# Kernel optimization log

Measured on AMD Instinct MI355X. Metric: run time of the kernel, lower is better.

The kernel has to match this reference:

```python
import jax, jax.numpy as jnp
import numpy as np

NB_VARS = 2_000_000
N0 = 2 + 2 * NB_VARS      # input vector length: [zero, one, pos0, neg0, pos1, neg1, ...]
M0 = 4_000_000            # prod layer 0 outputs (binary fan-in)
M1 = 1_000_000            # sum  layer 1 outputs (irregular fan-in)
M2 = 500_000              # prod layer 2 outputs (binary fan-in)
M3 = 125_000              # sum  layer 3 outputs (irregular fan-in)


def setup_inputs() -> dict:
    key = jax.random.key(0)
    ks = jax.random.split(key, 7)
    x_pos = jax.random.uniform(ks[0], (NB_VARS,), dtype=jnp.float32)
    ix_in0 = jax.random.randint(ks[1], (2 * M0,), 0, N0)            # edges of prod layer 0
    ix_in1 = jax.random.randint(ks[2], (8_000_000,), 0, M0)         # edges of sum layer 1
    ix_out1 = jnp.sort(jax.random.randint(ks[3], (8_000_000,), 0, M1))
    ix_in2 = jax.random.randint(ks[4], (2 * M2,), 0, M1)            # edges of prod layer 2
    ix_in3 = jax.random.randint(ks[5], (1_000_000,), 0, M2)         # edges of sum layer 3
    ix_out3 = jnp.sort(jax.random.randint(ks[6], (1_000_000,), 0, M3))
    return {"x_pos": x_pos, "ix_in0": ix_in0, "ix_in1": ix_in1, "ix_out1": ix_out1,
            "ix_in2": ix_in2, "ix_in3": ix_in3, "ix_out3": ix_out3}


def reference(x_pos, ix_in0, ix_in1, ix_out1, ix_in2, ix_in3, ix_out3):
    # encode_input (real semiring): neg = negate(pos) = 1 - pos; interleave; prepend [zero=0, one=1]
    neg = 1.0 - x_pos
    units = jnp.array([0.0, 1.0], dtype=x_pos.dtype)
    x = jnp.concatenate([units, jnp.stack([x_pos, neg], axis=1).reshape(-1)])  # [N0]

    # layer 0: product layer, binary fan-in -> gather + pairwise multiply
    e0 = x[ix_in0].reshape(M0, 2)
    x = e0[:, 0] * e0[:, 1]                                                    # [M0]

    # layer 1: sum layer, irregular fan-in -> gather + segment-sum
    x = jax.ops.segment_sum(x[ix_in1], ix_out1, num_segments=M1)               # [M1]

    # layer 2: product layer, binary fan-in
    e2 = x[ix_in2].reshape(M2, 2)
    x = e2[:, 0] * e2[:, 1]                                                    # [M2]

    # layer 3: sum layer, irregular fan-in
    x = jax.ops.segment_sum(x[ix_in3], ix_out3, num_segments=M3)               # [M3]
    return x
```

## Files before the change

### kernel.cpp

```cpp
#include <hip/hip_runtime.h>
#include <hip/hip_fp16.h>


#define PERS_BLOCKS 2048
#define PERS_THREADS 256
#define WBITS_H 20

typedef __attribute__((ext_vector_type(4))) int   iv4;
typedef __attribute__((ext_vector_type(4))) float fv4;
typedef __attribute__((ext_vector_type(4))) unsigned int uv4;

__device__ __forceinline__ iv4 nt_load4(const int* p) {
    return __builtin_nontemporal_load((const iv4*)p);
}

__global__ void init_kernel(const float* __restrict__ in, unsigned int* __restrict__ x16,
                            float* __restrict__ y1, float* __restrict__ out,
                            int n4, int nz1, int nzo) {
    int t = blockIdx.x * blockDim.x + threadIdx.x;
    if (t < n4) {
        fv4 f = __builtin_nontemporal_load((const fv4*)(in + 4 * (size_t)t));
        __half2 lo = __floats2half2_rn(f.x, f.y);
        __half2 hi = __floats2half2_rn(f.z, f.w);
        unsigned int rlo = *(const unsigned int*)&lo;
        unsigned int rhi = *(const unsigned int*)&hi;
        x16[2 * t]     = rlo;
        x16[2 * t + 1] = rhi;
    }
    if (t < nz1) {
        fv4 z = {0.f, 0.f, 0.f, 0.f};
        __builtin_nontemporal_store(z, (fv4*)(y1 + 4 * (size_t)t));
    }
    if (t < nzo) {
        fv4 z = {0.f, 0.f, 0.f, 0.f};
        __builtin_nontemporal_store(z, (fv4*)(out + 4 * (size_t)t));
    }
}

__device__ __forceinline__ float decode16(const __half* __restrict__ xp, int idx) {
    int k = (idx - 2) >> 1;
    k = k < 0 ? 0 : k;
    float v = __half2float(xp[k]);
    v = (idx & 1) ? 1.0f - v : v;
    if (idx < 2) v = (float)idx;
    return v;
}

__global__ void layer0_prod8_kernel(const __half* __restrict__ x16,
                                    const int* __restrict__ ix,
                                    unsigned int* __restrict__ out16, int nT) {
    int t = blockIdx.x * blockDim.x + threadIdx.x;
    if (t >= nT) return;
    iv4 p0 = nt_load4(ix + 16 * (size_t)t);
    iv4 p1 = nt_load4(ix + 16 * (size_t)t + 4);
    iv4 p2 = nt_load4(ix + 16 * (size_t)t + 8);
    iv4 p3 = nt_load4(ix + 16 * (size_t)t + 12);
    float a0 = decode16(x16, p0.x), b0 = decode16(x16, p0.y);
    float a1 = decode16(x16, p0.z), b1 = decode16(x16, p0.w);
    float a2 = decode16(x16, p1.x), b2 = decode16(x16, p1.y);
    float a3 = decode16(x16, p1.z), b3 = decode16(x16, p1.w);
    float a4 = decode16(x16, p2.x), b4 = decode16(x16, p2.y);
    float a5 = decode16(x16, p2.z), b5 = decode16(x16, p2.w);
    float a6 = decode16(x16, p3.x), b6 = decode16(x16, p3.y);
    float a7 = decode16(x16, p3.z), b7 = decode16(x16, p3.w);
    __half2 h0 = __floats2half2_rn(a0 * b0, a1 * b1);
    __half2 h1 = __floats2half2_rn(a2 * b2, a3 * b3);
    __half2 h2 = __floats2half2_rn(a4 * b4, a5 * b5);
    __half2 h3 = __floats2half2_rn(a6 * b6, a7 * b7);
    uv4 r;
    r.x = *(const unsigned int*)&h0;
    r.y = *(const unsigned int*)&h1;
    r.z = *(const unsigned int*)&h2;
    r.w = *(const unsigned int*)&h3;
    __builtin_nontemporal_store(r, (uv4*)(out16 + 4 * (size_t)t));
}

template<int NS, int NWIN>
__global__ __launch_bounds__(PERS_THREADS)
void sum_win_h_kernel(const __half* __restrict__ vin,
                      const int* __restrict__ ix_in,
                      const int* __restrict__ ix_out,
                      float* __restrict__ out, int nT4) {
    const int nTh  = gridDim.x * blockDim.x;
    const int gtid = blockIdx.x * blockDim.x + threadIdx.x;
    const int lane = threadIdx.x & 63;

    iv4    a[NS];
    iv4    sg[NS];
    float4 v[NS];
    bool   act[NS];
    #pragma unroll
    for (int s = 0; s < NS; ++s) {
        int t = s * nTh + gtid;
        act[s] = (t < nT4);
        if (act[s]) {
            a[s]  = nt_load4(ix_in  + 4 * (size_t)t);
            sg[s] = nt_load4(ix_out + 4 * (size_t)t);
        } else {
            a[s]  = (iv4){-1, -1, -1, -1};
            sg[s] = (iv4){-1, -1, -1, -1};
        }
        v[s] = make_float4(0.f, 0.f, 0.f, 0.f);
    }

    #pragma unroll
    for (int w = 0; w < NWIN; ++w) {
        #pragma unroll
        for (int s = 0; s < NS; ++s) {
            if ((a[s].x >> WBITS_H) == w) v[s].x = __half2float(vin[a[s].x]);
            if ((a[s].y >> WBITS_H) == w) v[s].y = __half2float(vin[a[s].y]);
            if ((a[s].z >> WBITS_H) == w) v[s].z = __half2float(vin[a[s].z]);
            if ((a[s].w >> WBITS_H) == w) v[s].w = __half2float(vin[a[s].w]);
        }
    }

    #pragma unroll
    for (int s = 0; s < NS; ++s) {
        int seg = -1; float val = 0.f;
        if (act[s]) {
            int cur = sg[s].x; float acc = v[s].x;
            if (sg[s].y == cur) acc += v[s].y; else { atomicAdd(&out[cur], acc); cur = sg[s].y; acc = v[s].y; }
            if (sg[s].z == cur) acc += v[s].z; else { atomicAdd(&out[cur], acc); cur = sg[s].z; acc = v[s].z; }
            if (sg[s].w == cur) acc += v[s].w; else { atomicAdd(&out[cur], acc); cur = sg[s].w; acc = v[s].w; }
            seg = cur; val = acc;
        }
        #pragma unroll
        for (int off = 1; off < 64; off <<= 1) {
            float vv = __shfl_up(val, off, 64);
            int   ss = __shfl_up(seg, off, 64);
            if (lane >= off && ss == seg) val += vv;
        }
        int seg_next = __shfl_down(seg, 1, 64);
        bool is_last = (lane == 63) || (seg_next != seg);
        if (act[s] && is_last) atomicAdd(&out[seg], val);
    }
}

__global__ void sum4_f32_kernel(const float* __restrict__ vin,
                                const int* __restrict__ ix_in,
                                const int* __restrict__ ix_out,
                                float* __restrict__ out, int nT4) {
    int t = blockIdx.x * blockDim.x + threadIdx.x;
    int lane = threadIdx.x & 63;
    int seg = -1; float val = 0.f;
    if (t < nT4) {
        iv4 a  = nt_load4(ix_in  + 4 * (size_t)t);
        iv4 sg = nt_load4(ix_out + 4 * (size_t)t);
        float v0 = vin[a.x], v1 = vin[a.y], v2 = vin[a.z], v3 = vin[a.w];
        int cur = sg.x; float acc = v0;
        if (sg.y == cur) acc += v1; else { atomicAdd(&out[cur], acc); cur = sg.y; acc = v1; }
        if (sg.z == cur) acc += v2; else { atomicAdd(&out[cur], acc); cur = sg.z; acc = v2; }
        if (sg.w == cur) acc += v3; else { atomicAdd(&out[cur], acc); cur = sg.w; acc = v3; }
        seg = cur; val = acc;
    }
    #pragma unroll
    for (int off = 1; off < 64; off <<= 1) {
        float vv = __shfl_up(val, off, 64);
        int   ss = __shfl_up(seg, off, 64);
        if (lane >= off && ss == seg) val += vv;
    }
    int seg_next = __shfl_down(seg, 1, 64);
    bool is_last = (lane == 63) || (seg_next != seg);
    if (t < nT4 && is_last) atomicAdd(&out[seg], val);
}

__global__ void prod2_kernel(const float* __restrict__ vin,
                             const int* __restrict__ ix,
                             float2* __restrict__ out, int nT) {
    int t = blockIdx.x * blockDim.x + threadIdx.x;
    if (t >= nT) return;
    iv4 p = nt_load4(ix + 4 * (size_t)t);
    float a0 = vin[p.x], b0 = vin[p.y];
    float a1 = vin[p.z], b1 = vin[p.w];
    float2 r; r.x = a0 * b0; r.y = a1 * b1;
    out[t] = r;
}

extern "C" void kernel_launch(void* const* d_in, const int* in_sizes, int n_in,
                              void* d_out, int out_size, void* d_ws, size_t ws_size,
                              hipStream_t stream) {
    const float* x_pos  = (const float*)d_in[0];
    const int*   ix_in0 = (const int*)d_in[1];
    const int*   ix_in1 = (const int*)d_in[2];
    const int*   ix_out1= (const int*)d_in[3];
    const int*   ix_in2 = (const int*)d_in[4];
    const int*   ix_in3 = (const int*)d_in[5];
    const int*   ix_out3= (const int*)d_in[6];
    float* out = (float*)d_out;

    const int NV = in_sizes[0];
    const int M0 = in_sizes[1] / 2;
    const int E1 = in_sizes[2];
    const int M1 = 1000000;
    const int M2 = in_sizes[4] / 2;
    const int E3 = in_sizes[5];
    const int M3 = out_size;

    char* ws = (char*)d_ws;
    __half* y0  = (__half*)(ws);
    float*  y1  = (float*)(ws + (size_t)8  * 1024 * 1024);
    float*  y2  = (float*)(ws + (size_t)12 * 1024 * 1024);
    __half* x16 = (__half*)(ws + (size_t)14 * 1024 * 1024);

    const int B = 256;

    int n4  = NV / 4;
    int nz1 = M1 / 4;
    int nzo = M3 / 4;
    init_kernel<<<(n4 + B - 1) / B, B, 0, stream>>>(
        x_pos, (unsigned int*)x16, y1, out, n4, nz1, nzo);

    int t0 = M0 / 8;
    layer0_prod8_kernel<<<(t0 + B - 1) / B, B, 0, stream>>>(
        x16, ix_in0, (unsigned int*)y0, t0);

    int t1 = E1 / 4;
    sum_win_h_kernel<4, 4><<<PERS_BLOCKS, PERS_THREADS, 0, stream>>>(
        y0, ix_in1, ix_out1, y1, t1);

    int t2 = M2 / 2;
    prod2_kernel<<<(t2 + B - 1) / B, B, 0, stream>>>(
        y1, ix_in2, (float2*)y2, t2);

    int t3 = E3 / 4;
    sum4_f32_kernel<<<(t3 + B - 1) / B, B, 0, stream>>>(
        y2, ix_in3, ix_out3, out, t3);
}
```

Before: 252.6 us.

## Fuse all layers into one cooperative persistent kernel with grid syncs

Replaces the five separate kernel launches with a single cooperative mega-kernel that runs each layer as a grid-stride phase separated by grid.sync(). The aim is to remove per-launch overhead and the tail idle time between kernels. The original multi-launch path stays as a fallback if the cooperative launch fails. In exchange it adds grid-wide barrier costs, an occupancy query on every call, and fixed grid sizing for every phase, which may lower per-phase parallelism compared with the tuned launches.

Result: slower. 759.7 us (+200.7%).

```diff
diff --git a/kernel.cpp b/kernel.cpp
--- a/kernel.cpp
+++ b/kernel.cpp
@@ -1,9 +1,11 @@
 #include <hip/hip_runtime.h>
 #include <hip/hip_fp16.h>
-
-
-#define PERS_BLOCKS 2048
-#define PERS_THREADS 256
+#include <hip/hip_cooperative_groups.h>
+
+namespace cg = cooperative_groups;
+
+
+#define NTHR 256
 #define WBITS_H 20
 
 typedef __attribute__((ext_vector_type(4))) int   iv4;
@@ -12,6 +14,183 @@
 
 __device__ __forceinline__ iv4 nt_load4(const int* p) {
     return __builtin_nontemporal_load((const iv4*)p);
+}
+
+__device__ __forceinline__ float decode16(const __half* __restrict__ xp, int idx) {
+    int k = (idx - 2) >> 1;
+    k = k < 0 ? 0 : k;
+    float v = __half2float(xp[k]);
+    v = (idx & 1) ? 1.0f - v : v;
+    if (idx < 2) v = (float)idx;
+    return v;
+}
+
+__global__ __launch_bounds__(NTHR, 8)
+void mega_kernel(const float* __restrict__ x_pos,
+                 const int* __restrict__ ix_in0,
+                 const int* __restrict__ ix_in1,
+                 const int* __restrict__ ix_out1,
+                 const int* __restrict__ ix_in2,
+                 const int* __restrict__ ix_in3,
+                 const int* __restrict__ ix_out3,
+                 float* __restrict__ out,
+                 __half* __restrict__ y0,
+                 float* __restrict__ y1,
+                 float* __restrict__ y2,
+                 __half* __restrict__ x16,
+                 int NV, int M0, int E1, int M1, int M2, int E3, int M3) {
+    cg::grid_group grid = cg::this_grid();
+    const int nTh  = gridDim.x * blockDim.x;
+    const int gtid = blockIdx.x * blockDim.x + threadIdx.x;
+    const int lane = threadIdx.x & 63;
+
+    {
+        int n4 = NV / 4;
+        for (int t = gtid; t < n4; t += nTh) {
+            fv4 f = __builtin_nontemporal_load((const fv4*)(x_pos + 4 * (size_t)t));
+            __half2 lo = __floats2half2_rn(f.x, f.y);
+            __half2 hi = __floats2half2_rn(f.z, f.w);
+            unsigned int* xu = (unsigned int*)x16;
+            xu[2 * t]     = *(const unsigned int*)&lo;
+            xu[2 * t + 1] = *(const unsigned int*)&hi;
+        }
+        int nz1 = M1 / 4;
+        for (int t = gtid; t < nz1; t += nTh) {
+            fv4 z = {0.f, 0.f, 0.f, 0.f};
+            __builtin_nontemporal_store(z, (fv4*)(y1 + 4 * (size_t)t));
+        }
+        int nzo = M3 / 4;
+        for (int t = gtid; t < nzo; t += nTh) {
+            fv4 z = {0.f, 0.f, 0.f, 0.f};
+            __builtin_nontemporal_store(z, (fv4*)(out + 4 * (size_t)t));
+        }
+    }
+    grid.sync();
+
+    {
+        int nT = M0 / 8;
+        for (int t = gtid; t < nT; t += nTh) {
+            iv4 p0 = nt_load4(ix_in0 + 16 * (size_t)t);
+            iv4 p1 = nt_load4(ix_in0 + 16 * (size_t)t + 4);
+            iv4 p2 = nt_load4(ix_in0 + 16 * (size_t)t + 8);
+            iv4 p3 = nt_load4(ix_in0 + 16 * (size_t)t + 12);
+            float a0 = decode16(x16, p0.x), b0 = decode16(x16, p0.y);
+            float a1 = decode16(x16, p0.z), b1 = decode16(x16, p0.w);
+            float a2 = decode16(x16, p1.x), b2 = decode16(x16, p1.y);
+            float a3 = decode16(x16, p1.z), b3 = decode16(x16, p1.w);
+            float a4 = decode16(x16, p2.x), b4 = decode16(x16, p2.y);
+            float a5 = decode16(x16, p2.z), b5 = decode16(x16, p2.w);
+            float a6 = decode16(x16, p3.x), b6 = decode16(x16, p3.y);
+            float a7 = decode16(x16, p3.z), b7 = decode16(x16, p3.w);
+            __half2 h0 = __floats2half2_rn(a0 * b0, a1 * b1);
+            __half2 h1 = __floats2half2_rn(a2 * b2, a3 * b3);
+            __half2 h2 = __floats2half2_rn(a4 * b4, a5 * b5);
+            __half2 h3 = __floats2half2_rn(a6 * b6, a7 * b7);
+            uv4 r;
+            r.x = *(const unsigned int*)&h0;
+            r.y = *(const unsigned int*)&h1;
+            r.z = *(const unsigned int*)&h2;
+            r.w = *(const unsigned int*)&h3;
+            __builtin_nontemporal_store(r, (uv4*)((unsigned int*)y0 + 4 * (size_t)t));
+        }
+    }
+    grid.sync();
+
+    {
+        const int NS = 4, NWIN = 4;
+        int nT4 = E1 / 4;
+        iv4    a[NS];
+        float4 v[NS];
+        bool   act[NS];
+        #pragma unroll
+        for (int s = 0; s < NS; ++s) {
+            int t = s * nTh + gtid;
+            act[s] = (t < nT4);
+            a[s] = act[s] ? nt_load4(ix_in1 + 4 * (size_t)t) : (iv4){-1, -1, -1, -1};
+            v[s] = make_float4(0.f, 0.f, 0.f, 0.f);
+        }
+        #pragma unroll
+        for (int w = 0; w < NWIN; ++w) {
+            #pragma unroll
+            for (int s = 0; s < NS; ++s) {
+                if ((a[s].x >> WBITS_H) == w) v[s].x = __half2float(y0[a[s].x]);
+                if ((a[s].y >> WBITS_H) == w) v[s].y = __half2float(y0[a[s].y]);
+                if ((a[s].z >> WBITS_H) == w) v[s].z = __half2float(y0[a[s].z]);
+                if ((a[s].w >> WBITS_H) == w) v[s].w = __half2float(y0[a[s].w]);
+            }
+        }
+        #pragma unroll
+        for (int s = 0; s < NS; ++s) {
+            int seg = -1; float val = 0.f;
+            if (act[s]) {
+                int t = s * nTh + gtid;
+                iv4 sg = nt_load4(ix_out1 + 4 * (size_t)t);
+                int cur = sg.x; float acc = v[s].x;
+                if (sg.y == cur) acc += v[s].y; else { atomicAdd(&y1[cur], acc); cur = sg.y; acc = v[s].y; }
+                if (sg.z == cur) acc += v[s].z; else { atomicAdd(&y1[cur], acc); cur = sg.z; acc = v[s].z; }
+                if (sg.w == cur) acc += v[s].w; else { atomicAdd(&y1[cur], acc); cur = sg.w; acc = v[s].w; }
+                seg = cur; val = acc;
+            }
+            #pragma unroll
+            for (int off = 1; off < 64; off <<= 1) {
+                float vv = __shfl_up(val, off, 64);
+                int   ss = __shfl_up(seg, off, 64);
+                if (lane >= off && ss == seg) val += vv;
+            }
+            int seg_next = __shfl_down(seg, 1, 64);
+            bool is_last = (lane == 63) || (seg_next != seg);
+            if (seg >= 0 && is_last) atomicAdd(&y1[seg], val);
+        }
+        for (int t = NS * nTh + gtid; t < nT4; t += nTh) {
+            iv4 at = nt_load4(ix_in1 + 4 * (size_t)t);
+            iv4 sg = nt_load4(ix_out1 + 4 * (size_t)t);
+            float v0 = __half2float(y0[at.x]);
+            float v1 = __half2float(y0[at.y]);
+            float v2 = __half2float(y0[at.z]);
+            float v3 = __half2float(y0[at.w]);
+            int cur = sg.x; float acc = v0;
+            if (sg.y == cur) acc += v1; else { atomicAdd(&y1[cur], acc); cur = sg.y; acc = v1; }
+            if (sg.z == cur) acc += v2; else { atomicAdd(&y1[cur], acc); cur = sg.z; acc = v2; }
+            if (sg.w == cur) acc += v3; else { atomicAdd(&y1[cur], acc); cur = sg.w; acc = v3; }
+            atomicAdd(&y1[cur], acc);
+        }
+    }
+    grid.sync();
+
+    {
+        int nT = M2 / 2;
+        for (int t = gtid; t < nT; t += nTh) {
+            iv4 p = nt_load4(ix_in2 + 4 * (size_t)t);
+            float a0 = y1[p.x], b0 = y1[p.y];
+            float a1 = y1[p.z], b1 = y1[p.w];
+            float2 r; r.x = a0 * b0; r.y = a1 * b1;
+            *(float2*)(y2 + 2 * (size_t)t) = r;
+        }
+    }
+    grid.sync();
+
+    {
+        int nT4 = E3 / 4;
+        for (int t = gtid; t < nT4; t += nTh) {
+            iv4 a  = nt_load4(ix_in3  + 4 * (size_t)t);
+            iv4 sg = nt_load4(ix_out3 + 4 * (size_t)t);
+            float v0 = y2[a.x], v1 = y2[a.y], v2 = y2[a.z], v3 = y2[a.w];
+            int cur = sg.x; float acc = v0;
+            if (sg.y == cur) acc += v1; else { atomicAdd(&out[cur], acc); cur = sg.y; acc = v1; }
+            if (sg.z == cur) acc += v2; else { atomicAdd(&out[cur], acc); cur = sg.z; acc = v2; }
+            if (sg.w == cur) acc += v3; else { atomicAdd(&out[cur], acc); cur = sg.w; acc = v3; }
+            int seg = cur; float val = acc;
+            #pragma unroll
+            for (int off = 1; off < 64; off <<= 1) {
+                float vv = __shfl_up(val, off, 64);
+                int   ss = __shfl_up(seg, off, 64);
+                if (lane >= off && ss == seg) val += vv;
+            }
+            int seg_next = __shfl_down(seg, 1, 64);
+            bool is_last = (lane == 63) || (seg_next != seg);
+            if (is_last) atomicAdd(&out[seg], val);
+        }
+    }
 }
 
 __global__ void init_kernel(const float* __restrict__ in, unsigned int* __restrict__ x16,
@@ -22,10 +201,8 @@
         fv4 f = __builtin_nontemporal_load((const fv4*)(in + 4 * (size_t)t));
         __half2 lo = __floats2half2_rn(f.x, f.y);
         __half2 hi = __floats2half2_rn(f.z, f.w);
-        unsigned int rlo = *(const unsigned int*)&lo;
-        unsigned int rhi = *(const unsigned int*)&hi;
-        x16[2 * t]     = rlo;
-        x16[2 * t + 1] = rhi;
+        x16[2 * t]     = *(const unsigned int*)&lo;
+        x16[2 * t + 1] = *(const unsigned int*)&hi;
     }
     if (t < nz1) {
         fv4 z = {0.f, 0.f, 0.f, 0.f};
@@ -35,15 +212,6 @@
         fv4 z = {0.f, 0.f, 0.f, 0.f};
         __builtin_nontemporal_store(z, (fv4*)(out + 4 * (size_t)t));
     }
-}
-
-__device__ __forceinline__ float decode16(const __half* __restrict__ xp, int idx) {
-    int k = (idx - 2) >> 1;
-    k = k < 0 ? 0 : k;
-    float v = __half2float(xp[k]);
-    v = (idx & 1) ? 1.0f - v : v;
-    if (idx < 2) v = (float)idx;
-    return v;
 }
 
 __global__ void layer0_prod8_kernel(const __half* __restrict__ x16,
@@ -76,7 +244,7 @@
 }
 
 template<int NS, int NWIN>
-__global__ __launch_bounds__(PERS_THREADS)
+__global__ __launch_bounds__(NTHR)
 void sum_win_h_kernel(const __half* __restrict__ vin,
                       const int* __restrict__ ix_in,
                       const int* __restrict__ ix_out,
@@ -102,7 +270,6 @@
         }
         v[s] = make_float4(0.f, 0.f, 0.f, 0.f);
     }
-
     #pragma unroll
     for (int w = 0; w < NWIN; ++w) {
         #pragma unroll
@@ -113,7 +280,6 @@
             if ((a[s].w >> WBITS_H) == w) v[s].w = __half2float(vin[a[s].w]);
         }
     }
-
     #pragma unroll
     for (int s = 0; s < NS; ++s) {
         int seg = -1; float val = 0.f;
@@ -188,13 +354,13 @@
     const int*   ix_out3= (const int*)d_in[6];
     float* out = (float*)d_out;
 
-    const int NV = in_sizes[0];
-    const int M0 = in_sizes[1] / 2;
-    const int E1 = in_sizes[2];
-    const int M1 = 1000000;
-    const int M2 = in_sizes[4] / 2;
-    const int E3 = in_sizes[5];
-    const int M3 = out_size;
+    int NV = in_sizes[0];
+    int M0 = in_sizes[1] / 2;
+    int E1 = in_sizes[2];
+    int M1 = 1000000;
+    int M2 = in_sizes[4] / 2;
+    int E3 = in_sizes[5];
+    int M3 = out_size;
 
     char* ws = (char*)d_ws;
     __half* y0  = (__half*)(ws);
@@ -202,8 +368,26 @@
     float*  y2  = (float*)(ws + (size_t)12 * 1024 * 1024);
     __half* x16 = (__half*)(ws + (size_t)14 * 1024 * 1024);
 
+    int blocksPerCU = 0;
+    hipError_t qerr = hipOccupancyMaxActiveBlocksPerMultiprocessor(
+        &blocksPerCU, (const void*)mega_kernel, NTHR, 0);
+    if (qerr != hipSuccess || blocksPerCU < 1) blocksPerCU = 1;
+    int nBlk = blocksPerCU * 256;
+    if (nBlk > 2048) nBlk = 2048;
+
+    void* args[] = {
+        (void*)&x_pos, (void*)&ix_in0, (void*)&ix_in1, (void*)&ix_out1,
+        (void*)&ix_in2, (void*)&ix_in3, (void*)&ix_out3, (void*)&out,
+        (void*)&y0, (void*)&y1, (void*)&y2, (void*)&x16,
+        (void*)&NV, (void*)&M0, (void*)&E1, (void*)&M1,
+        (void*)&M2, (void*)&E3, (void*)&M3,
+    };
+    hipError_t lerr = hipLaunchCooperativeKernel(
+        (const void*)mega_kernel, dim3(nBlk), dim3(NTHR), args, 0, stream);
+
+    if (lerr == hipSuccess) return;
+
     const int B = 256;
-
     int n4  = NV / 4;
     int nz1 = M1 / 4;
     int nzo = M3 / 4;
@@ -215,7 +399,7 @@
         x16, ix_in0, (unsigned int*)y0, t0);
 
     int t1 = E1 / 4;
-    sum_win_h_kernel<4, 4><<<PERS_BLOCKS, PERS_THREADS, 0, stream>>>(
+    sum_win_h_kernel<4, 4><<<2048, NTHR, 0, stream>>>(
         y0, ix_in1, ix_out1, y1, t1);
 
     int t2 = M2 / 2;
```

## Fuse input encode into layer0 and fuse layer2 product into layer3 sum

Applied to the files above, without the earlier changes.

Drops the fp16 conversion pass over x_pos so layer 0 gathers fp32 inputs directly, and folds the zero-init into the layer-0 kernel. Layer 2's product kernel is removed: layer 3 now gathers the ix_in2 pair for each edge and recomputes the product on the fly. This removes two launches and the y2/x16 round trips. In exchange, layer-0 gathers read a 2x larger fp32 table, and layer-2 products are recomputed once per layer-3 edge (1M edges vs 500K nodes) with dependent gathers.

After: 290.0 us. +14.8%, slower.

```diff
diff --git a/kernel.cpp b/kernel.cpp
--- a/kernel.cpp
+++ b/kernel.cpp
@@ -2,31 +2,36 @@
 #include <hip/hip_fp16.h>
 
 
-#define PERS_BLOCKS 2048
-#define PERS_THREADS 256
+#define NTHR 256
 #define WBITS_H 20
 
 typedef __attribute__((ext_vector_type(4))) int   iv4;
+typedef __attribute__((ext_vector_type(2))) int   iv2;
 typedef __attribute__((ext_vector_type(4))) float fv4;
 typedef __attribute__((ext_vector_type(4))) unsigned int uv4;
 
 __device__ __forceinline__ iv4 nt_load4(const int* p) {
     return __builtin_nontemporal_load((const iv4*)p);
 }
-
-__global__ void init_kernel(const float* __restrict__ in, unsigned int* __restrict__ x16,
-                            float* __restrict__ y1, float* __restrict__ out,
-                            int n4, int nz1, int nzo) {
+__device__ __forceinline__ iv2 nt_load2(const int* p) {
+    return __builtin_nontemporal_load((const iv2*)p);
+}
+
+__device__ __forceinline__ float decodef(const float* __restrict__ xp, int idx) {
+    int k = (idx - 2) >> 1;
+    k = k < 0 ? 0 : k;
+    float v = xp[k];
+    v = (idx & 1) ? 1.0f - v : v;
+    if (idx < 2) v = (float)idx;
+    return v;
+}
+
+__global__ void l0_fused_kernel(const float* __restrict__ x_pos,
+                                const int* __restrict__ ix,
+                                unsigned int* __restrict__ out16,
+                                float* __restrict__ y1, float* __restrict__ out,
+                                int nT, int nz1, int nzo) {
     int t = blockIdx.x * blockDim.x + threadIdx.x;
-    if (t < n4) {
-        fv4 f = __builtin_nontemporal_load((const fv4*)(in + 4 * (size_t)t));
-        __half2 lo = __floats2half2_rn(f.x, f.y);
-        __half2 hi = __floats2half2_rn(f.z, f.w);
-        unsigned int rlo = *(const unsigned int*)&lo;
-        unsigned int rhi = *(const unsigned int*)&hi;
-        x16[2 * t]     = rlo;
-        x16[2 * t + 1] = rhi;
-    }
     if (t < nz1) {
         fv4 z = {0.f, 0.f, 0.f, 0.f};
         __builtin_nontemporal_store(z, (fv4*)(y1 + 4 * (size_t)t));
@@ -35,34 +40,19 @@
         fv4 z = {0.f, 0.f, 0.f, 0.f};
         __builtin_nontemporal_store(z, (fv4*)(out + 4 * (size_t)t));
     }
-}
-
-__device__ __forceinline__ float decode16(const __half* __restrict__ xp, int idx) {
-    int k = (idx - 2) >> 1;
-    k = k < 0 ? 0 : k;
-    float v = __half2float(xp[k]);
-    v = (idx & 1) ? 1.0f - v : v;
-    if (idx < 2) v = (float)idx;
-    return v;
-}
-
-__global__ void layer0_prod8_kernel(const __half* __restrict__ x16,
-                                    const int* __restrict__ ix,
-                                    unsigned int* __restrict__ out16, int nT) {
-    int t = blockIdx.x * blockDim.x + threadIdx.x;
     if (t >= nT) return;
     iv4 p0 = nt_load4(ix + 16 * (size_t)t);
     iv4 p1 = nt_load4(ix + 16 * (size_t)t + 4);
     iv4 p2 = nt_load4(ix + 16 * (size_t)t + 8);
     iv4 p3 = nt_load4(ix + 16 * (size_t)t + 12);
-    float a0 = decode16(x16, p0.x), b0 = decode16(x16, p0.y);
-    float a1 = decode16(x16, p0.z), b1 = decode16(x16, p0.w);
-    float a2 = decode16(x16, p1.x), b2 = decode16(x16, p1.y);
-    float a3 = decode16(x16, p1.z), b3 = decode16(x16, p1.w);
-    float a4 = decode16(x16, p2.x), b4 = decode16(x16, p2.y);
-    float a5 = decode16(x16, p2.z), b5 = decode16(x16, p2.w);
-    float a6 = decode16(x16, p3.x), b6 = decode16(x16, p3.y);
-    float a7 = decode16(x16, p3.z), b7 = decode16(x16, p3.w);
+    float a0 = decodef(x_pos, p0.x), b0 = decodef(x_pos, p0.y);
+    float a1 = decodef(x_pos, p0.z), b1 = decodef(x_pos, p0.w);
+    float a2 = decodef(x_pos, p1.x), b2 = decodef(x_pos, p1.y);
+    float a3 = decodef(x_pos, p1.z), b3 = decodef(x_pos, p1.w);
+    float a4 = decodef(x_pos, p2.x), b4 = decodef(x_pos, p2.y);
+    float a5 = decodef(x_pos, p2.z), b5 = decodef(x_pos, p2.w);
+    float a6 = decodef(x_pos, p3.x), b6 = decodef(x_pos, p3.y);
+    float a7 = decodef(x_pos, p3.z), b7 = decodef(x_pos, p3.w);
     __half2 h0 = __floats2half2_rn(a0 * b0, a1 * b1);
     __half2 h1 = __floats2half2_rn(a2 * b2, a3 * b3);
     __half2 h2 = __floats2half2_rn(a4 * b4, a5 * b5);
@@ -76,7 +66,7 @@
 }
 
 template<int NS, int NWIN>
-__global__ __launch_bounds__(PERS_THREADS)
+__global__ __launch_bounds__(NTHR)
 void sum_win_h_kernel(const __half* __restrict__ vin,
                       const int* __restrict__ ix_in,
                       const int* __restrict__ ix_out,
@@ -102,7 +92,6 @@
         }
         v[s] = make_float4(0.f, 0.f, 0.f, 0.f);
     }
-
     #pragma unroll
     for (int w = 0; w < NWIN; ++w) {
         #pragma unroll
@@ -113,7 +102,6 @@
             if ((a[s].w >> WBITS_H) == w) v[s].w = __half2float(vin[a[s].w]);
         }
     }
-
     #pragma unroll
     for (int s = 0; s < NS; ++s) {
         int seg = -1; float val = 0.f;
@@ -136,17 +124,25 @@
     }
 }
 
-__global__ void sum4_f32_kernel(const float* __restrict__ vin,
-                                const int* __restrict__ ix_in,
-                                const int* __restrict__ ix_out,
-                                float* __restrict__ out, int nT4) {
+__global__ void l2l3_fused_kernel(const float* __restrict__ y1,
+                                  const int* __restrict__ ix_in2,
+                                  const int* __restrict__ ix_in3,
+                                  const int* __restrict__ ix_out3,
+                                  float* __restrict__ out, int nT4) {
     int t = blockIdx.x * blockDim.x + threadIdx.x;
     int lane = threadIdx.x & 63;
     int seg = -1; float val = 0.f;
     if (t < nT4) {
-        iv4 a  = nt_load4(ix_in  + 4 * (size_t)t);
-        iv4 sg = nt_load4(ix_out + 4 * (size_t)t);
-        float v0 = vin[a.x], v1 = vin[a.y], v2 = vin[a.z], v3 = vin[a.w];
+        iv4 e  = nt_load4(ix_in3  + 4 * (size_t)t);
+        iv4 sg = nt_load4(ix_out3 + 4 * (size_t)t);
+        iv2 q0 = nt_load2(ix_in2 + 2 * (size_t)e.x);
+        iv2 q1 = nt_load2(ix_in2 + 2 * (size_t)e.y);
+        iv2 q2 = nt_load2(ix_in2 + 2 * (size_t)e.z);
+        iv2 q3 = nt_load2(ix_in2 + 2 * (size_t)e.w);
+        float v0 = y1[q0.x] * y1[q0.y];
+        float v1 = y1[q1.x] * y1[q1.y];
+        float v2 = y1[q2.x] * y1[q2.y];
+        float v3 = y1[q3.x] * y1[q3.y];
         int cur = sg.x; float acc = v0;
         if (sg.y == cur) acc += v1; else { atomicAdd(&out[cur], acc); cur = sg.y; acc = v1; }
         if (sg.z == cur) acc += v2; else { atomicAdd(&out[cur], acc); cur = sg.z; acc = v2; }
@@ -162,18 +158,6 @@
     int seg_next = __shfl_down(seg, 1, 64);
     bool is_last = (lane == 63) || (seg_next != seg);
     if (t < nT4 && is_last) atomicAdd(&out[seg], val);
-}
-
-__global__ void prod2_kernel(const float* __restrict__ vin,
-                             const int* __restrict__ ix,
-                             float2* __restrict__ out, int nT) {
-    int t = blockIdx.x * blockDim.x + threadIdx.x;
-    if (t >= nT) return;
-    iv4 p = nt_load4(ix + 4 * (size_t)t);
-    float a0 = vin[p.x], b0 = vin[p.y];
-    float a1 = vin[p.z], b1 = vin[p.w];
-    float2 r; r.x = a0 * b0; r.y = a1 * b1;
-    out[t] = r;
 }
 
 extern "C" void kernel_launch(void* const* d_in, const int* in_sizes, int n_in,
@@ -188,41 +172,29 @@
     const int*   ix_out3= (const int*)d_in[6];
     float* out = (float*)d_out;
 
-    const int NV = in_sizes[0];
     const int M0 = in_sizes[1] / 2;
     const int E1 = in_sizes[2];
     const int M1 = 1000000;
-    const int M2 = in_sizes[4] / 2;
     const int E3 = in_sizes[5];
     const int M3 = out_size;
 
     char* ws = (char*)d_ws;
-    __half* y0  = (__half*)(ws);
-    float*  y1  = (float*)(ws + (size_t)8  * 1024 * 1024);
-    float*  y2  = (float*)(ws + (size_t)12 * 1024 * 1024);
-    __half* x16 = (__half*)(ws + (size_t)14 * 1024 * 1024);
-
-    const int B = 256;
-
-    int n4  = NV / 4;
+    __half* y0 = (__half*)(ws);
+    float*  y1 = (float*)(ws + (size_t)8 * 1024 * 1024);
+
+    const int B = NTHR;
+
+    int t0  = M0 / 8;
     int nz1 = M1 / 4;
     int nzo = M3 / 4;
-    init_kernel<<<(n4 + B - 1) / B, B, 0, stream>>>(
-        x_pos, (unsigned int*)x16, y1, out, n4, nz1, nzo);
-
-    int t0 = M0 / 8;
-    layer0_prod8_kernel<<<(t0 + B - 1) / B, B, 0, stream>>>(
-        x16, ix_in0, (unsigned int*)y0, t0);
+    l0_fused_kernel<<<(t0 + B - 1) / B, B, 0, stream>>>(
+        x_pos, ix_in0, (unsigned int*)y0, y1, out, t0, nz1, nzo);
 
     int t1 = E1 / 4;
-    sum_win_h_kernel<4, 4><<<PERS_BLOCKS, PERS_THREADS, 0, stream>>>(
+    sum_win_h_kernel<4, 4><<<2048, B, 0, stream>>>(
         y0, ix_in1, ix_out1, y1, t1);
 
-    int t2 = M2 / 2;
-    prod2_kernel<<<(t2 + B - 1) / B, B, 0, stream>>>(
-        y1, ix_in2, (float2*)y2, t2);
-
     int t3 = E3 / 4;
-    sum4_f32_kernel<<<(t3 + B - 1) / B, B, 0, stream>>>(
-        y2, ix_in3, ix_out3, out, t3);
-}
+    l2l3_fused_kernel<<<(t3 + B - 1) / B, B, 0, stream>>>(
+        y1, ix_in2, ix_in3, ix_out3, out, t3);
+}
```
